# Kernel tuning notes

Measured on AMD Instinct MI355X. Metric: run time of the kernel, lower is better.

## Reference

```python
import jax, jax.numpy as jnp
import numpy as np
from jax import lax

D_IN, HIDDEN, B, T = 64, 512, 256, 256


def _lstm_layer(x, W_ih, W_hh, b_ih, b_hh):
    """PyTorch-convention LSTM layer. x: [B, T, in]. Returns (ys [B,T,H], h_last [B,H]).
    Gate order i, f, g, o; gates = x W_ih^T + h W_hh^T + b_ih + b_hh."""
    Bb = x.shape[0]
    H = W_hh.shape[1]
    # precompute input projection for all timesteps: [T, B, 4H]
    xg = jnp.einsum('bti,gi->tbg', x, W_ih) + (b_ih + b_hh)
    h0 = jnp.zeros((Bb, H), dtype=x.dtype)
    c0 = jnp.zeros((Bb, H), dtype=x.dtype)

    def step(carry, xg_t):
        h, c = carry
        gates = xg_t + h @ W_hh.T  # [B, 4H]
        i, f, g, o = jnp.split(gates, 4, axis=-1)
        i = jax.nn.sigmoid(i)
        f = jax.nn.sigmoid(f)
        g = jnp.tanh(g)
        o = jax.nn.sigmoid(o)
        c = f * c + i * g
        h = o * jnp.tanh(c)
        return (h, c), h

    (h_last, _), ys = lax.scan(step, (h0, c0), xg)
    return ys.transpose(1, 0, 2), h_last


def setup_inputs() -> dict:
    key = jax.random.key(0)
    ks = jax.random.split(key, 12)
    s0 = 1.0 / np.sqrt(HIDDEN)  # PyTorch default init scale
    u = lambda k, shp: jax.random.uniform(k, shp, jnp.float32, -s0, s0)
    return {
        'x': jax.random.normal(ks[0], (B, T, D_IN), jnp.float32),
        'W_ih0': u(ks[1], (4 * HIDDEN, D_IN)),
        'W_hh0': u(ks[2], (4 * HIDDEN, HIDDEN)),
        'b_ih0': u(ks[3], (4 * HIDDEN,)),
        'b_hh0': u(ks[4], (4 * HIDDEN,)),
        'W_ih1': u(ks[5], (4 * HIDDEN, HIDDEN)),
        'W_hh1': u(ks[6], (4 * HIDDEN, HIDDEN)),
        'b_ih1': u(ks[7], (4 * HIDDEN,)),
        'b_hh1': u(ks[8], (4 * HIDDEN,)),
        'head_w': u(ks[9], (1, HIDDEN)),
        'head_b': u(ks[10], (1,)),
    }


def reference(x, W_ih0, W_hh0, b_ih0, b_hh0, W_ih1, W_hh1, b_ih1, b_hh1, head_w, head_b):
    ys0, _ = _lstm_layer(x, W_ih0, W_hh0, b_ih0, b_hh0)          # [B, T, H]
    _, h_last = _lstm_layer(ys0, W_ih1, W_hh1, b_ih1, b_hh1)    # only last step used
    out = h_last @ head_w.T + head_b                              # [B, 1]
    return out[:, 0]                                              # squeeze(-1) -> [B]
```

## Files before the change

### kernel.cpp

```cpp
#include <hip/hip_runtime.h>

#define HID 512
#define NB  256
#define TT  256
#define DIN 64
#define HBUF 131072
#define SLOT_SH HBUF
#define NSLOT 8

typedef __attribute__((ext_vector_type(8))) short short8;
typedef __attribute__((ext_vector_type(4))) float f32x4;

__device__ __forceinline__ unsigned short f2bf(float f) {
    unsigned int u = __float_as_uint(f);
    u += 0x7FFF + ((u >> 16) & 1);
    return (unsigned short)(u >> 16);
}
__device__ __forceinline__ float bf2f(unsigned short h) {
    return __uint_as_float(((unsigned int)h) << 16);
}

__device__ __forceinline__ float fsig(float x) {
    return __builtin_amdgcn_rcpf(1.f + __expf(-x));
}
__device__ __forceinline__ float ftanh(float x) {
    return 1.f - 2.f * __builtin_amdgcn_rcpf(1.f + __expf(2.f * x));
}

__device__ __forceinline__ void st_u32_llc(unsigned* p, unsigned v) {
    asm volatile("global_store_dword %0, %1, off sc0 sc1" :: "v"(p), "v"(v) : "memory");
}
__device__ __forceinline__ unsigned ld_u32_llc(const unsigned* p) {
    unsigned v;
    asm volatile("global_load_dword %0, %1, off sc0 sc1\n\ts_waitcnt vmcnt(0)"
                 : "=v"(v) : "v"(p) : "memory");
    return v;
}

#define MFMA1(acc, a, b) acc = __builtin_amdgcn_mfma_f32_16x16x32_bf16(a, b, acc, 0, 0, 0)

#define SW0_F 36
#define SW1_F 64
#define SW0_N (SW0_F * 512)
#define SW1_N (SW1_F * 512)
#define LDS_BYTES ((SW0_N + SW1_N) * 2)

__device__ __forceinline__ void store_h_pair(unsigned short* buf, size_t hoff,
                                             unsigned short v, int l) {
    unsigned int hv = (unsigned int)v;
    unsigned int up = __shfl_down(hv, 1);
    if ((l & 1) == 0)
        st_u32_llc((unsigned*)(buf + hoff), hv | (up << 16));
}

__device__ __forceinline__ void cohort_wait(unsigned* fc, int l, int target) {
    unsigned* pa = fc + l;
    unsigned* pb = fc + 64 + l;
    while ((int)ld_u32_llc(pa) < target) __builtin_amdgcn_s_sleep(1);
    while ((int)ld_u32_llc(pb) < target) __builtin_amdgcn_s_sleep(1);
}

__device__ __forceinline__ void orbit_transpose(f32x4& v, int m) {
    { float a = (m & 1) ? v[0] : v[1]; float b = __shfl_xor(a, 4); if (m & 1) v[0] = b; else v[1] = b; }
    { float a = (m & 1) ? v[2] : v[3]; float b = __shfl_xor(a, 4); if (m & 1) v[2] = b; else v[3] = b; }
    { float a = (m & 2) ? v[0] : v[2]; float b = __shfl_xor(a, 8); if (m & 2) v[0] = b; else v[2] = b; }
    { float a = (m & 2) ? v[1] : v[3]; float b = __shfl_xor(a, 8); if (m & 2) v[1] = b; else v[3] = b; }
}

__global__ __launch_bounds__(512, 2) void lstm_persistent(
    const float* __restrict__ x,
    const float* __restrict__ Wih0, const float* __restrict__ Whh0,
    const float* __restrict__ bih0, const float* __restrict__ bhh0,
    const float* __restrict__ Wih1, const float* __restrict__ Whh1,
    const float* __restrict__ bih1, const float* __restrict__ bhh1,
    const float* __restrict__ headw, const float* __restrict__ headb,
    unsigned short* h0base, unsigned short* h1base,
    unsigned* gf, float* __restrict__ out)
{
    extern __shared__ unsigned short lds[];
    unsigned short* sW0 = lds;
    unsigned short* sW1 = lds + SW0_N;

    const int tid = threadIdx.x;
    const int l   = tid & 63;
    const int w   = tid >> 6;
    const int bt  = w >> 1;
    const int bf  = w & 1;
    const int bid = blockIdx.x;
    const int gq  = bid & 3;
    const int jb  = bid >> 2;

    const int cohort = gq * 4 + bt;
    unsigned* f0c = gf + cohort * 128;
    unsigned* f1c = gf + 2048 + cohort * 128;
    unsigned* f0sig = f0c + bf * 64 + jb;
    unsigned* f1sig = f1c + bf * 64 + jb;

    const int r16 = l & 15;
    const int ko  = (l >> 4) * 8;
    {
        const int nrow = (r16 >> 2) * HID + jb * 8 + (r16 & 3);
        for (int fi = w; fi < SW0_F; fi += 8) {
            const int kt = fi >> 1, bf_ = fi & 1;
            const int n = nrow + bf_ * 4;
            const float* src = (kt < 2) ? (Wih0 + (size_t)n * DIN + kt * 32 + ko)
                                        : (Whh0 + (size_t)n * HID + (kt - 2) * 32 + ko);
            float v[8];
            *(float4*)&v[0] = *(const float4*)src;
            *(float4*)&v[4] = *(const float4*)(src + 4);
            union { unsigned short u[8]; uint4 q; } pb;
            #pragma unroll
            for (int e = 0; e < 8; ++e) pb.u[e] = f2bf(v[e]);
            *(uint4*)&sW0[fi * 512 + l * 8] = pb.q;
        }
        for (int fi = w; fi < SW1_F; fi += 8) {
            const int kt = fi >> 1, bf_ = fi & 1;
            const int n = nrow + bf_ * 4;
            const float* src = (kt < 16) ? (Wih1 + (size_t)n * HID + kt * 32 + ko)
                                         : (Whh1 + (size_t)n * HID + (kt - 16) * 32 + ko);
            float v[8];
            *(float4*)&v[0] = *(const float4*)src;
            *(float4*)&v[4] = *(const float4*)(src + 4);
            union { unsigned short u[8]; uint4 q; } pb;
            #pragma unroll
            for (int e = 0; e < 8; ++e) pb.u[e] = f2bf(v[e]);
            *(uint4*)&sW1[fi * 512 + l * 8] = pb.q;
        }
    }

    float bias0[4], bias1[4];
    #pragma unroll
    for (int gi = 0; gi < 4; ++gi) {
        const int nn = gi * HID + jb * 8 + bf * 4 + (l & 3);
        bias0[gi] = bih0[nn] + bhh0[nn];
        bias1[gi] = bih1[nn] + bhh1[nn];
    }
    float c0 = 0.f, c1 = 0.f;

    const int m      = (l >> 2) & 3;
    const int b_in   = (l >> 4) * 4 + m;
    const int b_glob = gq * 64 + bt * 16 + b_in;
    const int j_glob = jb * 8 + bf * 4 + (l & 3);
    const size_t hoff = ((((size_t)(b_glob >> 4)) * 16 + (j_glob >> 5)) * 64
                         + ((b_glob & 15) | (((j_glob >> 3) & 3) << 4))) * 8 + (j_glob & 7);
    const int btg = gq * 4 + bt;

    const int xrow = gq * 64 + bt * 16 + (l & 15);
    float xv0[8], xv1[8];
    {
        const float* s0 = x + ((size_t)xrow * TT + 0) * DIN + ko;
        *(float4*)&xv0[0] = *(const float4*)s0;
        *(float4*)&xv0[4] = *(const float4*)(s0 + 4);
        *(float4*)&xv1[0] = *(const float4*)(s0 + 32);
        *(float4*)&xv1[4] = *(const float4*)(s0 + 36);
    }

    __syncthreads();

    const short8 bx0 = *(const short8*)&sW0[(0 * 2 + bf) * 512 + l * 8];
    const short8 bx1 = *(const short8*)&sW0[(1 * 2 + bf) * 512 + l * 8];

    for (int it = 0; it <= TT; ++it) {
        cohort_wait(f0c, l, it);

        const unsigned short* h0c = h0base + (size_t)((it + 7) & 7) * SLOT_SH;
        unsigned short* h0n       = h0base + (size_t)(it & 7) * SLOT_SH;
        const unsigned short* h1c = h1base + (size_t)((it + 6) & 7) * SLOT_SH;
        unsigned short* h1n       = h1base + (size_t)((it + 7) & 7) * SLOT_SH;

        f32x4 acc0[2] = {{0.f,0.f,0.f,0.f},{0.f,0.f,0.f,0.f}};
        f32x4 acc1[2] = {{0.f,0.f,0.f,0.f},{0.f,0.f,0.f,0.f}};

        short8 fAh[16];
        #pragma unroll
        for (int kt = 0; kt < 16; ++kt) {
            const size_t o = (((size_t)btg * 16 + kt) * 64 + l) * 8;
            fAh[kt] = *(const short8*)&h0c[o];
        }

        if (it < TT) {
            {
                union { unsigned short u[8]; short8 s; } ah, al;
                #pragma unroll
                for (int e = 0; e < 8; ++e) {
                    unsigned short h = f2bf(xv0[e]);
                    ah.u[e] = h; al.u[e] = f2bf(xv0[e] - bf2f(h));
                }
                MFMA1(acc0[0], ah.s, bx0);
                MFMA1(acc0[0], al.s, bx0);
                #pragma unroll
                for (int e = 0; e < 8; ++e) {
                    unsigned short h = f2bf(xv1[e]);
                    ah.u[e] = h; al.u[e] = f2bf(xv1[e] - bf2f(h));
                }
                MFMA1(acc0[1], ah.s, bx1);
                MFMA1(acc0[1], al.s, bx1);
            }
            #pragma unroll
            for (int kt = 0; kt < 16; ++kt) {
                short8 b = *(const short8*)&sW0[((kt + 2) * 2 + bf) * 512 + l * 8];
                MFMA1(acc0[kt & 1], fAh[kt], b);
            }
            {
                f32x4 v = acc0[0] + acc0[1];
                orbit_transpose(v, m);
                const float iG = fsig(v[0] + bias0[0]);
                const float fG = fsig(v[1] + bias0[1]);
                const float gT = ftanh(v[2] + bias0[2]);
                const float oG = fsig(v[3] + bias0[3]);
                c0 = fmaf(fG, c0, iG * gT);
                const float h = oG * ftanh(c0);
                store_h_pair(h0n, hoff, f2bf(h), l);
            }
            asm volatile("s_waitcnt vmcnt(0)" ::: "memory");
            if (l == 0) st_u32_llc(f0sig, (unsigned)(it + 1));
        }

        if (it + 1 < TT) {
            const float* s0 = x + ((size_t)xrow * TT + (it + 1)) * DIN + ko;
            *(float4*)&xv0[0] = *(const float4*)s0;
            *(float4*)&xv0[4] = *(const float4*)(s0 + 4);
            *(float4*)&xv1[0] = *(const float4*)(s0 + 32);
            *(float4*)&xv1[4] = *(const float4*)(s0 + 36);
        }

        if (it > 0) {
            #pragma unroll
            for (int kt = 0; kt < 16; ++kt) {
                short8 b = *(const short8*)&sW1[(kt * 2 + bf) * 512 + l * 8];
                MFMA1(acc1[kt & 1], fAh[kt], b);
            }
        }

        cohort_wait(f1c, l, it);

        if (it > 0) {
            short8 fCh[16];
            #pragma unroll
            for (int kt = 0; kt < 16; ++kt) {
                const size_t o = (((size_t)btg * 16 + kt) * 64 + l) * 8;
                fCh[kt] = *(const short8*)&h1c[o];
            }
            #pragma unroll
            for (int kt = 0; kt < 16; ++kt) {
                short8 b = *(const short8*)&sW1[((16 + kt) * 2 + bf) * 512 + l * 8];
                MFMA1(acc1[kt & 1], fCh[kt], b);
            }
            {
                f32x4 v = acc1[0] + acc1[1];
                orbit_transpose(v, m);
                const float iG = fsig(v[0] + bias1[0]);
                const float fG = fsig(v[1] + bias1[1]);
                const float gT = ftanh(v[2] + bias1[2]);
                const float oG = fsig(v[3] + bias1[3]);
                c1 = fmaf(fG, c1, iG * gT);
                const float h = oG * ftanh(c1);
                store_h_pair(h1n, hoff, f2bf(h), l);
            }
        }
        asm volatile("s_waitcnt vmcnt(0)" ::: "memory");
        if (l == 0) st_u32_llc(f1sig, (unsigned)(it + 1));

        if ((it & 7) == 7) {
            __syncthreads();
            if (tid >= 448)
                __builtin_amdgcn_fence(__ATOMIC_ACQUIRE, "agent");
            __syncthreads();
        }
    }

    if (jb == 0) {
        {
            unsigned* hp = gf + 2048 + gq * 512 + tid;
            while ((int)ld_u32_llc(hp) < TT + 1) __builtin_amdgcn_s_sleep(1);
        }
        __syncthreads();
        const unsigned short* h1h = h1base + (size_t)((TT + 7) & 7) * SLOT_SH;
        const int bl_ = tid >> 3;
        const int qd  = tid & 7;
        const int b   = gq * 64 + bl_;
        const int btw = b >> 4;
        float s = 0.f;
        #pragma unroll
        for (int jt = qd * 2; jt < qd * 2 + 2; ++jt) {
            #pragma unroll
            for (int q2 = 0; q2 < 4; ++q2) {
                const size_t off = (((size_t)btw * 16 + jt) * 64 + ((b & 15) | (q2 << 4))) * 8;
                short8 vh = *(const short8*)&h1h[off];
                const int j0 = jt * 32 + q2 * 8;
                #pragma unroll
                for (int e = 0; e < 8; ++e)
                    s += bf2f((unsigned short)vh[e]) * headw[j0 + e];
            }
        }
        s += __shfl_down(s, 4, 8);
        s += __shfl_down(s, 2, 8);
        s += __shfl_down(s, 1, 8);
        if (qd == 0) out[b] = s + headb[0];
    }
}

extern "C" void kernel_launch(void* const* d_in, const int* in_sizes, int n_in,
                              void* d_out, int out_size, void* d_ws, size_t ws_size,
                              hipStream_t stream) {
    const float* x      = (const float*)d_in[0];
    const float* W_ih0  = (const float*)d_in[1];
    const float* W_hh0  = (const float*)d_in[2];
    const float* b_ih0  = (const float*)d_in[3];
    const float* b_hh0  = (const float*)d_in[4];
    const float* W_ih1  = (const float*)d_in[5];
    const float* W_hh1  = (const float*)d_in[6];
    const float* b_ih1  = (const float*)d_in[7];
    const float* b_hh1  = (const float*)d_in[8];
    const float* head_w = (const float*)d_in[9];
    const float* head_b = (const float*)d_in[10];
    float* out = (float*)d_out;

    const size_t SLOT_BYTES = (size_t)SLOT_SH * 2;
    unsigned* gf = (unsigned*)d_ws;
    unsigned short* h0base = (unsigned short*)((char*)d_ws + (1 << 20));
    unsigned short* h1base = (unsigned short*)((char*)d_ws + (1 << 20) + NSLOT * SLOT_BYTES);

    hipMemsetAsync(d_ws, 0, 16384, stream);
    hipMemsetAsync((char*)h0base + 7 * SLOT_BYTES, 0, SLOT_BYTES, stream);
    hipMemsetAsync((char*)h1base + 7 * SLOT_BYTES, 0, SLOT_BYTES, stream);

    hipFuncSetAttribute((const void*)lstm_persistent,
                        hipFuncAttributeMaxDynamicSharedMemorySize, LDS_BYTES);
    lstm_persistent<<<dim3(256), dim3(512), LDS_BYTES, stream>>>(
        x, W_ih0, W_hh0, b_ih0, b_hh0, W_ih1, W_hh1, b_ih1, b_hh1,
        head_w, head_b, h0base, h1base, gf, out);
}
```

Before: 1.545 ms.

## Split LSTM layers across dedicated warp groups with decoupled layer-0 lookahead

Waves in each block are split into two groups. Warps 0-3 compute layer 0 and warps 4-7 compute layer 1, with each wave covering both column halves instead of one. Layer 0 now waits only until layer 1 is within six steps, so it can run ahead, and the two per-cohort flag polls are merged into one dual-load spin. This is meant to take layer 0 off the serial critical path of layer 1, at the cost of more per-wave register pressure (launch bounds drop to one block per SIMD pair) and possibly unbalanced work between the two groups.

```diff
diff --git a/kernel.cpp b/kernel.cpp
--- a/kernel.cpp
+++ b/kernel.cpp
@@ -37,6 +37,19 @@
     return v;
 }
 
+__device__ __forceinline__ void dual_wait(const unsigned* pa, const unsigned* pb,
+                                          int ta, int tb) {
+    while (true) {
+        unsigned va, vb;
+        asm volatile("global_load_dword %0, %2, off sc0 sc1\n\t"
+                     "global_load_dword %1, %3, off sc0 sc1\n\t"
+                     "s_waitcnt vmcnt(0)"
+                     : "=&v"(va), "=&v"(vb) : "v"(pa), "v"(pb) : "memory");
+        if ((int)va >= ta && (int)vb >= tb) break;
+        __builtin_amdgcn_s_sleep(1);
+    }
+}
+
 #define MFMA1(acc, a, b) acc = __builtin_amdgcn_mfma_f32_16x16x32_bf16(a, b, acc, 0, 0, 0)
 
 #define SW0_F 36
@@ -53,13 +66,6 @@
         st_u32_llc((unsigned*)(buf + hoff), hv | (up << 16));
 }
 
-__device__ __forceinline__ void cohort_wait(unsigned* fc, int l, int target) {
-    unsigned* pa = fc + l;
-    unsigned* pb = fc + 64 + l;
-    while ((int)ld_u32_llc(pa) < target) __builtin_amdgcn_s_sleep(1);
-    while ((int)ld_u32_llc(pb) < target) __builtin_amdgcn_s_sleep(1);
-}
-
 __device__ __forceinline__ void orbit_transpose(f32x4& v, int m) {
     { float a = (m & 1) ? v[0] : v[1]; float b = __shfl_xor(a, 4); if (m & 1) v[0] = b; else v[1] = b; }
     { float a = (m & 1) ? v[2] : v[3]; float b = __shfl_xor(a, 4); if (m & 1) v[2] = b; else v[3] = b; }
@@ -67,7 +73,7 @@
     { float a = (m & 2) ? v[1] : v[3]; float b = __shfl_xor(a, 8); if (m & 2) v[1] = b; else v[3] = b; }
 }
 
-__global__ __launch_bounds__(512, 2) void lstm_persistent(
+__global__ __launch_bounds__(512, 1) void lstm_persistent(
     const float* __restrict__ x,
     const float* __restrict__ Wih0, const float* __restrict__ Whh0,
     const float* __restrict__ bih0, const float* __restrict__ bhh0,
@@ -84,17 +90,15 @@
     const int tid = threadIdx.x;
     const int l   = tid & 63;
     const int w   = tid >> 6;
-    const int bt  = w >> 1;
-    const int bf  = w & 1;
+    const int lw  = w >> 2;
+    const int bt  = w & 3;
     const int bid = blockIdx.x;
     const int gq  = bid & 3;
     const int jb  = bid >> 2;
 
     const int cohort = gq * 4 + bt;
-    unsigned* f0c = gf + cohort * 128;
-    unsigned* f1c = gf + 2048 + cohort * 128;
-    unsigned* f0sig = f0c + bf * 64 + jb;
-    unsigned* f1sig = f1c + bf * 64 + jb;
+    unsigned* f0c = gf + cohort * 64;
+    unsigned* f1c = gf + 1024 + cohort * 64;
 
     const int r16 = l & 15;
     const int ko  = (l >> 4) * 8;
@@ -128,150 +132,171 @@
         }
     }
 
-    float bias0[4], bias1[4];
+    const int m     = (l >> 2) & 3;
+    const int b_in  = (l >> 4) * 4 + m;
+    const int b_glob = gq * 64 + bt * 16 + b_in;
+    float biasA[2][4];
+    size_t hoffA[2];
     #pragma unroll
-    for (int gi = 0; gi < 4; ++gi) {
-        const int nn = gi * HID + jb * 8 + bf * 4 + (l & 3);
-        bias0[gi] = bih0[nn] + bhh0[nn];
-        bias1[gi] = bih1[nn] + bhh1[nn];
-    }
-    float c0 = 0.f, c1 = 0.f;
-
-    const int m      = (l >> 2) & 3;
-    const int b_in   = (l >> 4) * 4 + m;
-    const int b_glob = gq * 64 + bt * 16 + b_in;
-    const int j_glob = jb * 8 + bf * 4 + (l & 3);
-    const size_t hoff = ((((size_t)(b_glob >> 4)) * 16 + (j_glob >> 5)) * 64
-                         + ((b_glob & 15) | (((j_glob >> 3) & 3) << 4))) * 8 + (j_glob & 7);
+    for (int bf_ = 0; bf_ < 2; ++bf_) {
+        const int j_glob = jb * 8 + bf_ * 4 + (l & 3);
+        #pragma unroll
+        for (int gi = 0; gi < 4; ++gi) {
+            const int nn = gi * HID + jb * 8 + bf_ * 4 + (l & 3);
+            biasA[bf_][gi] = lw == 0 ? (bih0[nn] + bhh0[nn]) : (bih1[nn] + bhh1[nn]);
+        }
+        hoffA[bf_] = ((((size_t)(b_glob >> 4)) * 16 + (j_glob >> 5)) * 64
+                      + ((b_glob & 15) | (((j_glob >> 3) & 3) << 4))) * 8 + (j_glob & 7);
+    }
     const int btg = gq * 4 + bt;
 
-    const int xrow = gq * 64 + bt * 16 + (l & 15);
-    float xv0[8], xv1[8];
-    {
-        const float* s0 = x + ((size_t)xrow * TT + 0) * DIN + ko;
-        *(float4*)&xv0[0] = *(const float4*)s0;
-        *(float4*)&xv0[4] = *(const float4*)(s0 + 4);
-        *(float4*)&xv1[0] = *(const float4*)(s0 + 32);
-        *(float4*)&xv1[4] = *(const float4*)(s0 + 36);
-    }
-
     __syncthreads();
 
-    const short8 bx0 = *(const short8*)&sW0[(0 * 2 + bf) * 512 + l * 8];
-    const short8 bx1 = *(const short8*)&sW0[(1 * 2 + bf) * 512 + l * 8];
-
-    for (int it = 0; it <= TT; ++it) {
-        cohort_wait(f0c, l, it);
-
-        const unsigned short* h0c = h0base + (size_t)((it + 7) & 7) * SLOT_SH;
-        unsigned short* h0n       = h0base + (size_t)(it & 7) * SLOT_SH;
-        const unsigned short* h1c = h1base + (size_t)((it + 6) & 7) * SLOT_SH;
-        unsigned short* h1n       = h1base + (size_t)((it + 7) & 7) * SLOT_SH;
-
-        f32x4 acc0[2] = {{0.f,0.f,0.f,0.f},{0.f,0.f,0.f,0.f}};
-        f32x4 acc1[2] = {{0.f,0.f,0.f,0.f},{0.f,0.f,0.f,0.f}};
-
-        short8 fAh[16];
-        #pragma unroll
-        for (int kt = 0; kt < 16; ++kt) {
-            const size_t o = (((size_t)btg * 16 + kt) * 64 + l) * 8;
-            fAh[kt] = *(const short8*)&h0c[o];
-        }
-
-        if (it < TT) {
-            {
-                union { unsigned short u[8]; short8 s; } ah, al;
-                #pragma unroll
-                for (int e = 0; e < 8; ++e) {
-                    unsigned short h = f2bf(xv0[e]);
-                    ah.u[e] = h; al.u[e] = f2bf(xv0[e] - bf2f(h));
-                }
-                MFMA1(acc0[0], ah.s, bx0);
-                MFMA1(acc0[0], al.s, bx0);
-                #pragma unroll
-                for (int e = 0; e < 8; ++e) {
-                    unsigned short h = f2bf(xv1[e]);
-                    ah.u[e] = h; al.u[e] = f2bf(xv1[e] - bf2f(h));
-                }
-                MFMA1(acc0[1], ah.s, bx1);
-                MFMA1(acc0[1], al.s, bx1);
-            }
-            #pragma unroll
-            for (int kt = 0; kt < 16; ++kt) {
-                short8 b = *(const short8*)&sW0[((kt + 2) * 2 + bf) * 512 + l * 8];
-                MFMA1(acc0[kt & 1], fAh[kt], b);
-            }
-            {
-                f32x4 v = acc0[0] + acc0[1];
-                orbit_transpose(v, m);
-                const float iG = fsig(v[0] + bias0[0]);
-                const float fG = fsig(v[1] + bias0[1]);
-                const float gT = ftanh(v[2] + bias0[2]);
-                const float oG = fsig(v[3] + bias0[3]);
-                c0 = fmaf(fG, c0, iG * gT);
-                const float h = oG * ftanh(c0);
-                store_h_pair(h0n, hoff, f2bf(h), l);
-            }
-            asm volatile("s_waitcnt vmcnt(0)" ::: "memory");
-            if (l == 0) st_u32_llc(f0sig, (unsigned)(it + 1));
-        }
-
-        if (it + 1 < TT) {
-            const float* s0 = x + ((size_t)xrow * TT + (it + 1)) * DIN + ko;
+    if (lw == 0) {
+        const short8 bx[2][2] = {
+            { *(const short8*)&sW0[(0 * 2 + 0) * 512 + l * 8],
+              *(const short8*)&sW0[(1 * 2 + 0) * 512 + l * 8] },
+            { *(const short8*)&sW0[(0 * 2 + 1) * 512 + l * 8],
+              *(const short8*)&sW0[(1 * 2 + 1) * 512 + l * 8] } };
+        float c0[2] = {0.f, 0.f};
+        const int xrow = gq * 64 + bt * 16 + (l & 15);
+        float xv0[8], xv1[8];
+        {
+            const float* s0 = x + ((size_t)xrow * TT + 0) * DIN + ko;
             *(float4*)&xv0[0] = *(const float4*)s0;
             *(float4*)&xv0[4] = *(const float4*)(s0 + 4);
             *(float4*)&xv1[0] = *(const float4*)(s0 + 32);
             *(float4*)&xv1[4] = *(const float4*)(s0 + 36);
         }
 
-        if (it > 0) {
-            #pragma unroll
-            for (int kt = 0; kt < 16; ++kt) {
-                short8 b = *(const short8*)&sW1[(kt * 2 + bf) * 512 + l * 8];
-                MFMA1(acc1[kt & 1], fAh[kt], b);
-            }
-        }
-
-        cohort_wait(f1c, l, it);
-
-        if (it > 0) {
-            short8 fCh[16];
-            #pragma unroll
-            for (int kt = 0; kt < 16; ++kt) {
-                const size_t o = (((size_t)btg * 16 + kt) * 64 + l) * 8;
-                fCh[kt] = *(const short8*)&h1c[o];
-            }
-            #pragma unroll
-            for (int kt = 0; kt < 16; ++kt) {
-                short8 b = *(const short8*)&sW1[((16 + kt) * 2 + bf) * 512 + l * 8];
-                MFMA1(acc1[kt & 1], fCh[kt], b);
-            }
-            {
-                f32x4 v = acc1[0] + acc1[1];
-                orbit_transpose(v, m);
-                const float iG = fsig(v[0] + bias1[0]);
-                const float fG = fsig(v[1] + bias1[1]);
-                const float gT = ftanh(v[2] + bias1[2]);
-                const float oG = fsig(v[3] + bias1[3]);
-                c1 = fmaf(fG, c1, iG * gT);
-                const float h = oG * ftanh(c1);
-                store_h_pair(h1n, hoff, f2bf(h), l);
-            }
-        }
-        asm volatile("s_waitcnt vmcnt(0)" ::: "memory");
-        if (l == 0) st_u32_llc(f1sig, (unsigned)(it + 1));
-
-        if ((it & 7) == 7) {
-            __syncthreads();
-            if (tid >= 448)
-                __builtin_amdgcn_fence(__ATOMIC_ACQUIRE, "agent");
-            __syncthreads();
+        for (int it = 0; it <= TT; ++it) {
+            dual_wait(f0c + l, f1c + l, it, it - 6);
+
+            const unsigned short* h0c = h0base + (size_t)((it + 7) & 7) * SLOT_SH;
+            unsigned short* h0n       = h0base + (size_t)(it & 7) * SLOT_SH;
+
+            if (it < TT) {
+                f32x4 acc[2][2] = {{{0.f,0.f,0.f,0.f},{0.f,0.f,0.f,0.f}},
+                                   {{0.f,0.f,0.f,0.f},{0.f,0.f,0.f,0.f}}};
+                short8 fAh[16];
+                #pragma unroll
+                for (int kt = 0; kt < 16; ++kt) {
+                    const size_t o = (((size_t)btg * 16 + kt) * 64 + l) * 8;
+                    fAh[kt] = *(const short8*)&h0c[o];
+                }
+                {
+                    union { unsigned short u[8]; short8 s; } ah, al;
+                    #pragma unroll
+                    for (int e = 0; e < 8; ++e) {
+                        unsigned short h = f2bf(xv0[e]);
+                        ah.u[e] = h; al.u[e] = f2bf(xv0[e] - bf2f(h));
+                    }
+                    MFMA1(acc[0][0], ah.s, bx[0][0]); MFMA1(acc[0][0], al.s, bx[0][0]);
+                    MFMA1(acc[1][0], ah.s, bx[1][0]); MFMA1(acc[1][0], al.s, bx[1][0]);
+                    #pragma unroll
+                    for (int e = 0; e < 8; ++e) {
+                        unsigned short h = f2bf(xv1[e]);
+                        ah.u[e] = h; al.u[e] = f2bf(xv1[e] - bf2f(h));
+                    }
+                    MFMA1(acc[0][1], ah.s, bx[0][1]); MFMA1(acc[0][1], al.s, bx[0][1]);
+                    MFMA1(acc[1][1], ah.s, bx[1][1]); MFMA1(acc[1][1], al.s, bx[1][1]);
+                }
+                #pragma unroll
+                for (int kt = 0; kt < 16; ++kt) {
+                    short8 b0 = *(const short8*)&sW0[((kt + 2) * 2 + 0) * 512 + l * 8];
+                    short8 b1 = *(const short8*)&sW0[((kt + 2) * 2 + 1) * 512 + l * 8];
+                    MFMA1(acc[0][kt & 1], fAh[kt], b0);
+                    MFMA1(acc[1][kt & 1], fAh[kt], b1);
+                }
+                #pragma unroll
+                for (int bf_ = 0; bf_ < 2; ++bf_) {
+                    f32x4 v = acc[bf_][0] + acc[bf_][1];
+                    orbit_transpose(v, m);
+                    const float iG = fsig(v[0] + biasA[bf_][0]);
+                    const float fG = fsig(v[1] + biasA[bf_][1]);
+                    const float gT = ftanh(v[2] + biasA[bf_][2]);
+                    const float oG = fsig(v[3] + biasA[bf_][3]);
+                    c0[bf_] = fmaf(fG, c0[bf_], iG * gT);
+                    const float h = oG * ftanh(c0[bf_]);
+                    store_h_pair(h0n, hoffA[bf_], f2bf(h), l);
+                }
+                asm volatile("s_waitcnt vmcnt(0)" ::: "memory");
+                if (l == 0) st_u32_llc(f0c + jb, (unsigned)(it + 1));
+            }
+            if (it + 1 < TT) {
+                const float* s0 = x + ((size_t)xrow * TT + (it + 1)) * DIN + ko;
+                *(float4*)&xv0[0] = *(const float4*)s0;
+                *(float4*)&xv0[4] = *(const float4*)(s0 + 4);
+                *(float4*)&xv1[0] = *(const float4*)(s0 + 32);
+                *(float4*)&xv1[4] = *(const float4*)(s0 + 36);
+            }
+            if ((it & 7) == 7) {
+                __syncthreads();
+                __syncthreads();
+            }
+        }
+    } else {
+        float c1[2] = {0.f, 0.f};
+
+        for (int it = 0; it <= TT; ++it) {
+            dual_wait(f0c + l, f1c + l, it, it);
+
+            const unsigned short* h0c = h0base + (size_t)((it + 7) & 7) * SLOT_SH;
+            const unsigned short* h1c = h1base + (size_t)((it + 6) & 7) * SLOT_SH;
+            unsigned short* h1n       = h1base + (size_t)((it + 7) & 7) * SLOT_SH;
+
+            if (it > 0) {
+                f32x4 acc[2][2] = {{{0.f,0.f,0.f,0.f},{0.f,0.f,0.f,0.f}},
+                                   {{0.f,0.f,0.f,0.f},{0.f,0.f,0.f,0.f}}};
+                short8 fAh[16], fCh[16];
+                #pragma unroll
+                for (int kt = 0; kt < 16; ++kt) {
+                    const size_t o = (((size_t)btg * 16 + kt) * 64 + l) * 8;
+                    fAh[kt] = *(const short8*)&h0c[o];
+                    fCh[kt] = *(const short8*)&h1c[o];
+                }
+                #pragma unroll
+                for (int kt = 0; kt < 16; ++kt) {
+                    short8 b0 = *(const short8*)&sW1[(kt * 2 + 0) * 512 + l * 8];
+                    short8 b1 = *(const short8*)&sW1[(kt * 2 + 1) * 512 + l * 8];
+                    MFMA1(acc[0][kt & 1], fAh[kt], b0);
+                    MFMA1(acc[1][kt & 1], fAh[kt], b1);
+                }
+                #pragma unroll
+                for (int kt = 0; kt < 16; ++kt) {
+                    short8 b0 = *(const short8*)&sW1[((16 + kt) * 2 + 0) * 512 + l * 8];
+                    short8 b1 = *(const short8*)&sW1[((16 + kt) * 2 + 1) * 512 + l * 8];
+                    MFMA1(acc[0][kt & 1], fCh[kt], b0);
+                    MFMA1(acc[1][kt & 1], fCh[kt], b1);
+                }
+                #pragma unroll
+                for (int bf_ = 0; bf_ < 2; ++bf_) {
+                    f32x4 v = acc[bf_][0] + acc[bf_][1];
+                    orbit_transpose(v, m);
+                    const float iG = fsig(v[0] + biasA[bf_][0]);
+                    const float fG = fsig(v[1] + biasA[bf_][1]);
+                    const float gT = ftanh(v[2] + biasA[bf_][2]);
+                    const float oG = fsig(v[3] + biasA[bf_][3]);
+                    c1[bf_] = fmaf(fG, c1[bf_], iG * gT);
+                    const float h = oG * ftanh(c1[bf_]);
+                    store_h_pair(h1n, hoffA[bf_], f2bf(h), l);
+                }
+            }
+            asm volatile("s_waitcnt vmcnt(0)" ::: "memory");
+            if (l == 0) st_u32_llc(f1c + jb, (unsigned)(it + 1));
+
+            if ((it & 7) == 7) {
+                __syncthreads();
+                if (w == 7)
+                    __builtin_amdgcn_fence(__ATOMIC_ACQUIRE, "agent");
+                __syncthreads();
+            }
         }
     }
 
     if (jb == 0) {
-        {
-            unsigned* hp = gf + 2048 + gq * 512 + tid;
+        if (tid < 256) {
+            unsigned* hp = gf + 1024 + gq * 256 + tid;
             while ((int)ld_u32_llc(hp) < TT + 1) __builtin_amdgcn_s_sleep(1);
         }
         __syncthreads();
@@ -321,7 +346,7 @@
     unsigned short* h0base = (unsigned short*)((char*)d_ws + (1 << 20));
     unsigned short* h1base = (unsigned short*)((char*)d_ws + (1 << 20) + NSLOT * SLOT_BYTES);
 
-    hipMemsetAsync(d_ws, 0, 16384, stream);
+    hipMemsetAsync(d_ws, 0, 8192, stream);
     hipMemsetAsync((char*)h0base + 7 * SLOT_BYTES, 0, SLOT_BYTES, stream);
     hipMemsetAsync((char*)h1base + 7 * SLOT_BYTES, 0, SLOT_BYTES, stream);
 
```

Measured after the change: 4.806 ms. 211% more time.
